# Optimization experiments

Measured on AMD Instinct MI355X. Metric: run time of the kernel, lower is better.

## Reference

```python
import jax, jax.numpy as jnp
import numpy as np
from jax import lax

CIN, COUT, NCLS = 512, 256, 1
B, H, W = 4, 64, 64
EPS = 1e-5


def conv1x1(x, w):
    # x: [B,I,H,W], w: [O,I]
    return jnp.einsum('oi,bihw->bohw', w, x)


def conv3x3(x, w):
    # x: [B,I,H,W], w: [O,I,3,3], padding=1
    return lax.conv_general_dilated(x, w, (1, 1), 'SAME',
                                    dimension_numbers=('NCHW', 'OIHW', 'NCHW'))


def bn_relu(x, g, b):
    # training-mode BatchNorm2d (biased var over B,H,W) + ReLU
    mean = jnp.mean(x, axis=(0, 2, 3), keepdims=True)
    var = jnp.var(x, axis=(0, 2, 3), keepdims=True)
    xn = (x - mean) * lax.rsqrt(var + EPS)
    return jax.nn.relu(xn * g[None, :, None, None] + b[None, :, None, None])


def attention(xf, yf, wq, wk, wv, gamma):
    # cross-attn when yf != xf, self-attn when yf is xf; no 1/sqrt(d) scaling (faithful)
    Bb, C, Hh, Ww = xf.shape
    N = Hh * Ww
    q = conv1x1(xf, wq).reshape(Bb, C, N)
    k = conv1x1(yf, wk).reshape(Bb, C, N)
    v = conv1x1(yf, wv).reshape(Bb, C, N)
    att = jax.nn.softmax(jnp.einsum('bcn,bcm->bnm', q, k), axis=-1)  # [B,N,N]
    out = jnp.einsum('bcm,bnm->bcn', v, att).reshape(Bb, C, Hh, Ww)  # v @ att^T
    return gamma * out + xf


def setup_inputs() -> dict:
    key = jax.random.key(0)
    ks = jax.random.split(key, 16)
    Cs = COUT + 2

    def w(k, shape, fan_in):
        return jax.random.normal(k, shape, dtype=jnp.float32) / np.sqrt(fan_in)

    return {
        'x': jax.random.normal(ks[0], (B, CIN, H, W), dtype=jnp.float32),
        'y': jax.random.normal(ks[1], (B, CIN, H, W), dtype=jnp.float32),
        'flow': jax.random.normal(ks[2], (B, 2, H, W), dtype=jnp.float32),
        'w1x1': w(ks[3], (COUT, CIN), CIN),
        'b1x1': jnp.zeros((COUT,), dtype=jnp.float32),
        'ca_wq': w(ks[4], (COUT, COUT), COUT),
        'ca_wk': w(ks[5], (COUT, COUT), COUT),
        'ca_wv': w(ks[6], (COUT, COUT), COUT),
        'ca_gamma': jnp.full((1,), 0.1, dtype=jnp.float32),
        'cbr1_w': w(ks[7], (COUT, COUT, 3, 3), COUT * 9),
        'bn1_g': jnp.ones((COUT,), dtype=jnp.float32),
        'bn1_b': jnp.zeros((COUT,), dtype=jnp.float32),
        'sa_wq': w(ks[8], (Cs, Cs), Cs),
        'sa_wk': w(ks[9], (Cs, Cs), Cs),
        'sa_wv': w(ks[10], (Cs, Cs), Cs),
        'sa_gamma': jnp.full((1,), 0.1, dtype=jnp.float32),
        'cbr2_w': w(ks[11], (COUT, Cs, 3, 3), Cs * 9),
        'bn2_g': jnp.ones((COUT,), dtype=jnp.float32),
        'bn2_b': jnp.zeros((COUT,), dtype=jnp.float32),
        'pred_w': w(ks[12], (NCLS, COUT), COUT),
        'pred_b': jnp.zeros((NCLS,), dtype=jnp.float32),
    }


def reference(x, y, flow, w1x1, b1x1, ca_wq, ca_wk, ca_wv, ca_gamma,
              cbr1_w, bn1_g, bn1_b, sa_wq, sa_wk, sa_wv, sa_gamma,
              cbr2_w, bn2_g, bn2_b, pred_w, pred_b):
    xb = conv1x1(x, w1x1) + b1x1[None, :, None, None]
    yb = conv1x1(y, w1x1) + b1x1[None, :, None, None]
    t = attention(xb, yb, ca_wq, ca_wk, ca_wv, ca_gamma)
    cross_out = bn_relu(conv3x3(t, cbr1_w), bn1_g, bn1_b)
    cat = jnp.concatenate([cross_out, flow], axis=1)  # [B, COUT+2, H, W]
    t = attention(cat, cat, sa_wq, sa_wk, sa_wv, sa_gamma)
    t = bn_relu(conv3x3(t, cbr2_w), bn2_g, bn2_b)
    out = conv1x1(t, pred_w) + pred_b[None, :, None, None]
    return out
```

## Files before the change

### kernel.cpp

```cpp
#include <hip/hip_runtime.h>
#include <hip/hip_bf16.h>
#include <math.h>


#define NPIX 4096
#define NB   4

typedef __attribute__((ext_vector_type(8))) short short8v;
typedef __attribute__((ext_vector_type(4))) float float4v;

__device__ __forceinline__ short f2bs(float f) {
  __hip_bfloat16 h = __float2bfloat16(f);
  short r; __builtin_memcpy(&r, &h, 2); return r;
}

__device__ __forceinline__ void glld16(const void* g, void* l) {
  __builtin_amdgcn_global_load_lds(
      (const __attribute__((address_space(1))) unsigned int*)g,
      (__attribute__((address_space(3))) unsigned int*)l, 16, 0, 0);
}

__global__ __launch_bounds__(256) void transp_kernel(
    const float* __restrict__ X, __hip_bfloat16* __restrict__ XT)
{
  const int i0 = blockIdx.x * 64, n0 = blockIdx.y * 64, b = blockIdx.z;
  const int tid = threadIdx.x;
  __shared__ float Ls[64][68];
#pragma unroll
  for (int it = 0; it < 4; ++it) {
    int ir = it * 16 + (tid >> 4);
    int nc = (tid & 15) * 4;
    float4 v = *(const float4*)(X + ((size_t)b * 512 + i0 + ir) * NPIX + n0 + nc);
    *(float4*)(&Ls[ir][nc]) = v;
  }
  __syncthreads();
#pragma unroll
  for (int ot = 0; ot < 2; ++ot) {
    int n = ot * 32 + (tid >> 3);
    int ig = tid & 7;
    short8v o;
#pragma unroll
    for (int j = 0; j < 8; ++j) o[j] = f2bs(Ls[8 * ig + j][n]);
    *(short8v*)(XT + ((size_t)b * NPIX + n0 + n) * 512 + i0 + 8 * ig) = o;
  }
}

__global__ void wprep_kernel(const float* __restrict__ Win,
                             __hip_bfloat16* __restrict__ Wout,
                             int Or, int Ir, int Op, int Ip)
{
  size_t total = (size_t)Op * Ip;
  for (size_t e = (size_t)blockIdx.x * 256 + threadIdx.x; e < total;
       e += (size_t)gridDim.x * 256) {
    int i = (int)(e % Ip);
    int o = (int)(e / Ip);
    float v = (o < Or && i < Ir) ? Win[(size_t)o * Ir + i] : 0.f;
    Wout[e] = __float2bfloat16(v);
  }
}

__global__ void wtransbf_kernel(const float* __restrict__ Win,
                                __hip_bfloat16* __restrict__ Wout,
                                int O, int Ir, int Ip)
{
  size_t total = (size_t)9 * O * Ip;
  for (size_t e = (size_t)blockIdx.x * 256 + threadIdx.x; e < total;
       e += (size_t)gridDim.x * 256) {
    int i = (int)(e % Ip);
    size_t r = e / Ip;
    int o = (int)(r % O);
    int dydx = (int)(r / O);
    float v = (i < Ir) ? Win[((size_t)o * Ir + i) * 9 + dydx] : 0.f;
    Wout[e] = __float2bfloat16(v);
  }
}

template<int OMODE>
__global__ __launch_bounds__(256, 3) void gemm3_kernel(
    const __hip_bfloat16* __restrict__ X, const __hip_bfloat16* __restrict__ Wb,
    const float* __restrict__ Bias, float* __restrict__ Yf,
    __hip_bfloat16* __restrict__ Yb, int Ip, int O)
{
  const int n0 = blockIdx.x * 64, o0 = blockIdx.y * 64, b = blockIdx.z;
  const int tid = threadIdx.x, wv = tid >> 6, lane = tid & 63;
  const int lg = lane >> 4, lr = lane & 15;
  __shared__ __align__(16) __hip_bfloat16 Xs[64 * 32];
  __shared__ __align__(16) __hip_bfloat16 Wsh[64 * 32];

  const int nn = tid >> 2, ig = tid & 3;
  const __hip_bfloat16* xrow = X + ((size_t)b * NPIX + n0 + nn) * Ip;
  const __hip_bfloat16* wrow = Wb + (size_t)(o0 + nn) * Ip;
  const int sw = 8 * (ig ^ (nn & 3));

  float4v acc[4];
#pragma unroll
  for (int f = 0; f < 4; ++f) acc[f] = (float4v){0.f, 0.f, 0.f, 0.f};

  const int nch = Ip >> 5;
  short8v xr_ = *(const short8v*)(xrow + sw);
  short8v wr_ = *(const short8v*)(wrow + sw);

  for (int ci = 0; ci < nch; ++ci) {
    __syncthreads();
    *(short8v*)(Xs  + nn * 32 + ig * 8) = xr_;
    *(short8v*)(Wsh + nn * 32 + ig * 8) = wr_;
    __syncthreads();
    if (ci + 1 < nch) {
      xr_ = *(const short8v*)(xrow + (ci + 1) * 32 + sw);
      wr_ = *(const short8v*)(wrow + (ci + 1) * 32 + sw);
    }
    if (OMODE != 4) {
      int ar = 16 * wv + lr;
      short8v a = *(const short8v*)(Xs + ar * 32 + 8 * (lg ^ (ar & 3)));
#pragma unroll
      for (int of = 0; of < 4; ++of) {
        int br = 16 * of + lr;
        short8v bb = *(const short8v*)(Wsh + br * 32 + 8 * (lg ^ (br & 3)));
        acc[of] = __builtin_amdgcn_mfma_f32_16x16x32_bf16(a, bb, acc[of], 0, 0, 0);
      }
    } else {
      int ar = 16 * wv + lr;
      short8v a = *(const short8v*)(Wsh + ar * 32 + 8 * (lg ^ (ar & 3)));
#pragma unroll
      for (int nf = 0; nf < 4; ++nf) {
        int br = 16 * nf + lr;
        short8v bb = *(const short8v*)(Xs + br * 32 + 8 * (lg ^ (br & 3)));
        acc[nf] = __builtin_amdgcn_mfma_f32_16x16x32_bf16(a, bb, acc[nf], 0, 0, 0);
      }
    }
  }

  if (OMODE < 2) {
#pragma unroll
    for (int r = 0; r < 4; ++r) {
      size_t row = (size_t)b * NPIX + n0 + 16 * wv + 4 * lg + r;
#pragma unroll
      for (int of = 0; of < 4; ++of) {
        int o = o0 + 16 * of + lr;
        if (o < O) {
          float v = acc[of][r] + (Bias ? Bias[o] : 0.f);
          if (OMODE == 0) Yf[row * O + o] = v;
          Yb[row * O + o] = __float2bfloat16(v);
        }
      }
    }
  } else if (OMODE == 3) {
    __hip_bfloat16* Hb = Yb + (size_t)b * NPIX * O;
#pragma unroll
    for (int r = 0; r < 4; ++r) {
      size_t n = n0 + 16 * wv + 4 * lg + r;
#pragma unroll
      for (int of = 0; of < 4; ++of) {
        int o = o0 + 16 * of + lr;
        if (o < O)
          Hb[((size_t)(o >> 3) * NPIX + n) * 8 + (o & 7)] = __float2bfloat16(acc[of][r]);
      }
    }
  } else {
    __hip_bfloat16* Hb = Yb + (size_t)b * NPIX * O;
#pragma unroll
    for (int r = 0; r < 4; ++r) {
      int c = o0 + 16 * wv + 4 * lg + r;
      if (c < O) {
#pragma unroll
        for (int nf = 0; nf < 4; ++nf) {
          int n = n0 + 16 * nf + lr;
          Hb[((size_t)(n >> 3) * O + c) * 8 + (n & 7)] = __float2bfloat16(acc[nf][r]);
        }
      }
    }
  }
}

template<int C, int RF, int S>
__global__ __launch_bounds__(256, 2) void flash4_kernel(
    const __hip_bfloat16* __restrict__ Q, const __hip_bfloat16* __restrict__ K,
    const __hip_bfloat16* __restrict__ V,
    __hip_bfloat16* __restrict__ Opart, float* __restrict__ ml)
{
  constexpr int N    = NPIX;
  constexpr int NC32 = C / 32;
  constexpr int NCF  = C / 16;
  constexpr int QB   = 16 * RF;
  constexpr int KBYTES = 128 * C;
  constexpr int NT   = (N / S) / 64;

  __shared__ __align__(1024) char smem[256 * C];
  __hip_bfloat16* Ks = (__hip_bfloat16*)smem;
  __hip_bfloat16* Vs = (__hip_bfloat16*)(smem + KBYTES);
  __hip_bfloat16* Ps = (__hip_bfloat16*)smem;

  const int n0 = blockIdx.x * (4 * QB);
  const int split = blockIdx.y, b = blockIdx.z;
  const int tid = threadIdx.x, w = tid >> 6, lane = tid & 63;
  const int lg = lane >> 4, lr = lane & 15;

  const __hip_bfloat16* Kb = K + (size_t)b * N * C;
  const __hip_bfloat16* Vb = V + (size_t)b * N * C;

  short8v qf[RF][NC32];
#pragma unroll
  for (int rf = 0; rf < RF; ++rf) {
    const __hip_bfloat16* qp =
        Q + ((size_t)b * N + n0 + QB * w + 16 * rf + lr) * C + 8 * lg;
#pragma unroll
    for (int ks = 0; ks < NC32; ++ks) qf[rf][ks] = *(const short8v*)(qp + 32 * ks);
  }

  float4v oacc[RF][NCF];
#pragma unroll
  for (int rf = 0; rf < RF; ++rf)
#pragma unroll
    for (int f = 0; f < NCF; ++f) oacc[rf][f] = (float4v){0.f, 0.f, 0.f, 0.f};
  float mrun[RF][4], lrun[RF][4];
#pragma unroll
  for (int rf = 0; rf < RF; ++rf)
#pragma unroll
    for (int r = 0; r < 4; ++r) { mrun[rf][r] = -INFINITY; lrun[rf][r] = 0.f; }

  const int m0base = split * (N / S);

  for (int t = 0; t < NT; ++t) {
    const int m0 = m0base + t * 64;
    __syncthreads();
    for (int u = w; u < C / 8; u += 4)
      glld16(Kb + ((size_t)u * N + m0 + lane) * 8, Ks + u * 512);
    for (int u = w; u < C / 8; u += 4) {
      int s = u * 64 + lane;
      int kv8 = s / C, c = s % C;
      glld16(Vb + ((size_t)(m0 / 8 + kv8) * C + c) * 8, Vs + u * 512);
    }
    asm volatile("s_waitcnt vmcnt(0)" ::: "memory");
    __syncthreads();

    float4v sacc[RF][4];
#pragma unroll
    for (int rf = 0; rf < RF; ++rf)
#pragma unroll
      for (int mf = 0; mf < 4; ++mf) sacc[rf][mf] = (float4v){0.f, 0.f, 0.f, 0.f};
    __builtin_amdgcn_s_setprio(1);
#pragma unroll
    for (int ks = 0; ks < NC32; ++ks)
#pragma unroll
      for (int mf = 0; mf < 4; ++mf) {
        short8v kf = *(const short8v*)(Ks + ((4 * ks + lg) * 64 + 16 * mf + lr) * 8);
#pragma unroll
        for (int rf = 0; rf < RF; ++rf)
          sacc[rf][mf] =
              __builtin_amdgcn_mfma_f32_16x16x32_bf16(qf[rf][ks], kf, sacc[rf][mf], 0, 0, 0);
      }
    __builtin_amdgcn_s_setprio(0);
    __syncthreads();

    float scal[RF][4];
#pragma unroll
    for (int rf = 0; rf < RF; ++rf)
#pragma unroll
      for (int r = 0; r < 4; ++r) {
        float pm = fmaxf(fmaxf(sacc[rf][0][r], sacc[rf][1][r]),
                         fmaxf(sacc[rf][2][r], sacc[rf][3][r]));
#pragma unroll
        for (int off = 1; off < 16; off <<= 1) pm = fmaxf(pm, __shfl_xor(pm, off));
        float mnew = fmaxf(mrun[rf][r], pm);
        float sc = __expf(mrun[rf][r] - mnew);
        mrun[rf][r] = mnew;
        float rs = 0.f;
#pragma unroll
        for (int mf = 0; mf < 4; ++mf) {
          float p = __expf(sacc[rf][mf][r] - mnew);
          rs += p;
          Ps[(size_t)(w * QB + 16 * rf + 4 * lg + r) * 72 + 16 * mf + lr] =
              __float2bfloat16(p);
        }
#pragma unroll
        for (int off = 1; off < 16; off <<= 1) rs += __shfl_xor(rs, off);
        lrun[rf][r] = lrun[rf][r] * sc + rs;
        scal[rf][r] = sc;
      }
#pragma unroll
    for (int rf = 0; rf < RF; ++rf)
#pragma unroll
      for (int f = 0; f < NCF; ++f)
#pragma unroll
        for (int r = 0; r < 4; ++r) oacc[rf][f][r] *= scal[rf][r];

    asm volatile("s_waitcnt lgkmcnt(0)" ::: "memory");

    short8v pa[RF][2];
#pragma unroll
    for (int rf = 0; rf < RF; ++rf)
#pragma unroll
      for (int h = 0; h < 2; ++h)
        pa[rf][h] = *(const short8v*)(Ps + (size_t)(w * QB + 16 * rf + lr) * 72 +
                                      32 * h + 8 * lg);
    __builtin_amdgcn_s_setprio(1);
#pragma unroll
    for (int cf = 0; cf < NCF; ++cf)
#pragma unroll
      for (int h = 0; h < 2; ++h) {
        short8v vf = *(const short8v*)(Vs + ((h * 4 + lg) * C + 16 * cf + lr) * 8);
#pragma unroll
        for (int rf = 0; rf < RF; ++rf)
          oacc[rf][cf] =
              __builtin_amdgcn_mfma_f32_16x16x32_bf16(pa[rf][h], vf, oacc[rf][cf], 0, 0, 0);
      }
    __builtin_amdgcn_s_setprio(0);
  }

  const size_t rbase = (size_t)(split * NB + b) * N;
#pragma unroll
  for (int rf = 0; rf < RF; ++rf)
#pragma unroll
    for (int r = 0; r < 4; ++r) {
      int n = n0 + QB * w + 16 * rf + 4 * lg + r;
      if (lr == 0) {
        ml[(rbase + n) * 2]     = mrun[rf][r];
        ml[(rbase + n) * 2 + 1] = lrun[rf][r];
      }
#pragma unroll
      for (int cf = 0; cf < NCF; ++cf)
        Opart[(rbase + n) * C + 16 * cf + lr] = __float2bfloat16(oacc[rf][cf][r]);
    }
}

template<int C, int S>
__global__ __launch_bounds__(256) void merge4_kernel(
    const __hip_bfloat16* __restrict__ Op, const float* __restrict__ ml,
    const float* __restrict__ R, const float* __restrict__ gamma_p,
    __hip_bfloat16* __restrict__ T)
{
  const size_t row = blockIdx.x;
  float m = -INFINITY;
#pragma unroll
  for (int s = 0; s < S; ++s)
    m = fmaxf(m, ml[((size_t)s * NB * NPIX + row) * 2]);
  float e[S]; float L = 0.f;
#pragma unroll
  for (int s = 0; s < S; ++s) {
    e[s] = __expf(ml[((size_t)s * NB * NPIX + row) * 2] - m);
    L += ml[((size_t)s * NB * NPIX + row) * 2 + 1] * e[s];
  }
  float rinv = gamma_p[0] / L;
  for (int c = threadIdx.x; c < C; c += 256) {
    float o = 0.f;
#pragma unroll
    for (int s = 0; s < S; ++s)
      o += __bfloat162float(Op[((size_t)s * NB * NPIX + row) * C + c]) * e[s];
    T[row * C + c] = __float2bfloat16(o * rinv + R[row * C + c]);
  }
}

template<int IC>
__global__ __launch_bounds__(256, 2) void conv3_kernel(
    const __hip_bfloat16* __restrict__ X, const __hip_bfloat16* __restrict__ W2,
    float* __restrict__ Y)
{
  constexpr int NCH = IC / 32;
  constexpr int XP = 66 * 32;
  const int h = blockIdx.x, o0 = blockIdx.y * 64, b = blockIdx.z;
  const int tid = threadIdx.x, wv = tid >> 6, lane = tid & 63;
  const int lg = lane >> 4, lr = lane & 15;

  __shared__ __align__(16) __hip_bfloat16 Ws[9 * 64 * 32];
  __shared__ __align__(16) __hip_bfloat16 X3[3 * XP];

  for (int e = tid; e < 192; e += 256) {
    int p = e / 64, rr = (e >> 5) & 1, i = e & 31;
    X3[p * XP + (rr ? 65 * 32 : 0) + i] = __float2bfloat16(0.f);
  }

  float4v acc[4];
#pragma unroll
  for (int f = 0; f < 4; ++f) acc[f] = (float4v){0.f, 0.f, 0.f, 0.f};

  short8v xreg[3], wreg[9];
#define LOADX(CI)                                                              \
  _Pragma("unroll")                                                            \
  for (int j = 0; j < 3; ++j) {                                                \
    int s = tid + j * 256;                                                     \
    int dy = s >> 8, ww = (s >> 2) & 63, ig = s & 3;                           \
    int hs = h + dy - 1;                                                       \
    if (hs >= 0 && hs < 64)                                                    \
      xreg[j] = *(const short8v*)(X + ((size_t)b * NPIX + hs * 64 + ww) * IC + \
                                  (CI) * 32 + 8 * (ig ^ ((ww + 1) & 3)));      \
    else                                                                       \
      xreg[j] = (short8v){0, 0, 0, 0, 0, 0, 0, 0};                             \
  }
#define LOADW(CI)                                                              \
  _Pragma("unroll")                                                            \
  for (int j = 0; j < 9; ++j) {                                                \
    int s = tid + j * 256;                                                     \
    int dydx = s >> 8, oo = (s >> 2) & 63, ig = s & 3;                         \
    wreg[j] = *(const short8v*)(W2 + ((size_t)(dydx * 256 + o0 + oo)) * IC +   \
                                (CI) * 32 + 8 * (ig ^ (oo & 3)));              \
  }
  LOADX(0); LOADW(0);

  for (int ci = 0; ci < NCH; ++ci) {
    __syncthreads();
#pragma unroll
    for (int j = 0; j < 3; ++j) {
      int s = tid + j * 256;
      int dy = s >> 8, ww = (s >> 2) & 63, ig = s & 3;
      *(short8v*)(X3 + dy * XP + (ww + 1) * 32 + ig * 8) = xreg[j];
    }
#pragma unroll
    for (int j = 0; j < 9; ++j) {
      int s = tid + j * 256;
      *(short8v*)(Ws + s * 8) = wreg[j];
    }
    __syncthreads();
    if (ci + 1 < NCH) { LOADX(ci + 1); LOADW(ci + 1); }
#pragma unroll
    for (int dy = 0; dy < 3; ++dy)
#pragma unroll
      for (int dx = 0; dx < 3; ++dx) {
        int rs_ = 16 * wv + lr + dx;
        short8v a = *(const short8v*)(X3 + dy * XP + rs_ * 32 + 8 * (lg ^ (rs_ & 3)));
#pragma unroll
        for (int of = 0; of < 4; ++of) {
          int br = 16 * of + lr;
          short8v bb = *(const short8v*)(Ws + (dy * 3 + dx) * 2048 + br * 32 +
                                         8 * (lg ^ (br & 3)));
          acc[of] = __builtin_amdgcn_mfma_f32_16x16x32_bf16(a, bb, acc[of], 0, 0, 0);
        }
      }
  }
#pragma unroll
  for (int r = 0; r < 4; ++r) {
    size_t row = (size_t)b * NPIX + h * 64 + 16 * wv + 4 * lg + r;
#pragma unroll
    for (int of = 0; of < 4; ++of)
      Y[row * 256 + o0 + 16 * of + lr] = acc[of][r];
  }
#undef LOADX
#undef LOADW
}

__global__ __launch_bounds__(256) void stats1_kernel(
    const float* __restrict__ X, float* __restrict__ Part)
{
  const int o0 = (blockIdx.x & 3) * 64;
  const int rc = blockIdx.x >> 2;
  const int tid = threadIdx.x;
  const int o = o0 + (tid & 63), rq = tid >> 6;
  float s = 0.f, sq = 0.f;
  for (int rr = rq; rr < 256; rr += 4) {
    float v = X[(size_t)(rc * 256 + rr) * 256 + o];
    s += v; sq += v * v;
  }
  __shared__ float rs[256], rq2[256];
  rs[tid] = s; rq2[tid] = sq;
  __syncthreads();
  if (tid < 64) {
    s  = rs[tid] + rs[tid + 64] + rs[tid + 128] + rs[tid + 192];
    sq = rq2[tid] + rq2[tid + 64] + rq2[tid + 128] + rq2[tid + 192];
    Part[(o0 + tid) * 128 + rc * 2]     = s;
    Part[(o0 + tid) * 128 + rc * 2 + 1] = sq;
  }
}

__global__ __launch_bounds__(256) void stats2_kernel(
    const float* __restrict__ Part, float* __restrict__ Mean, float* __restrict__ Rstd)
{
  const int o = threadIdx.x;
  float s = 0.f, sq = 0.f;
  for (int rc = 0; rc < 64; ++rc) {
    s += Part[o * 128 + rc * 2];
    sq += Part[o * 128 + rc * 2 + 1];
  }
  float mean = s / 16384.f;
  float var = sq / 16384.f - mean * mean;
  Mean[o] = mean;
  Rstd[o] = 1.f / sqrtf(var + 1e-5f);
}

__global__ __launch_bounds__(320) void bnapply1_kernel(
    const float* __restrict__ X, const float* __restrict__ Flow,
    const float* __restrict__ Mean, const float* __restrict__ Rstd,
    const float* __restrict__ G, const float* __restrict__ Bt,
    float* __restrict__ CatF, __hip_bfloat16* __restrict__ CatB)
{
  const size_t row = blockIdx.x;
  const int t = threadIdx.x;
  if (t >= 288) return;
  float val;
  if (t < 256) {
    float v = X[row * 256 + t];
    val = fmaxf((v - Mean[t]) * Rstd[t] * G[t] + Bt[t], 0.f);
  } else if (t < 258) {
    int b = (int)(row >> 12), n = (int)(row & 4095);
    val = Flow[((size_t)(b * 2 + (t - 256)) << 12) + n];
  } else val = 0.f;
  CatF[row * 288 + t] = val;
  CatB[row * 288 + t] = __float2bfloat16(val);
}

__global__ __launch_bounds__(256) void bnapply2_kernel(
    float* X, const float* __restrict__ Mean, const float* __restrict__ Rstd,
    const float* __restrict__ G, const float* __restrict__ Bt)
{
  const size_t idx = (size_t)blockIdx.x * 256 + threadIdx.x;
  const int t = threadIdx.x;
  float v = X[idx];
  X[idx] = fmaxf((v - Mean[t]) * Rstd[t] * G[t] + Bt[t], 0.f);
}

__global__ __launch_bounds__(256) void pred3_kernel(
    const float* __restrict__ X, const float* __restrict__ Wp,
    const float* __restrict__ Bp, float* __restrict__ Out)
{
  const int wv = threadIdx.x >> 6, lane = threadIdx.x & 63;
  const size_t row = (size_t)blockIdx.x * 4 + wv;
  const float* xr = X + row * 256;
  float acc = 0.f;
#pragma unroll
  for (int cc = 0; cc < 4; ++cc) acc = fmaf(xr[cc * 64 + lane], Wp[cc * 64 + lane], acc);
#pragma unroll
  for (int off = 1; off < 64; off <<= 1) acc += __shfl_xor(acc, off);
  if (lane == 0) Out[row] = acc + Bp[0];
}

extern "C" void kernel_launch(void* const* d_in, const int* in_sizes, int n_in,
                              void* d_out, int out_size, void* d_ws, size_t ws_size,
                              hipStream_t stream)
{
  (void)in_sizes; (void)n_in; (void)out_size; (void)ws_size;
  const float* x      = (const float*)d_in[0];
  const float* y      = (const float*)d_in[1];
  const float* flow   = (const float*)d_in[2];
  const float* w1x1   = (const float*)d_in[3];
  const float* b1x1   = (const float*)d_in[4];
  const float* ca_wq  = (const float*)d_in[5];
  const float* ca_wk  = (const float*)d_in[6];
  const float* ca_wv  = (const float*)d_in[7];
  const float* ca_g   = (const float*)d_in[8];
  const float* cbr1_w = (const float*)d_in[9];
  const float* bn1_g  = (const float*)d_in[10];
  const float* bn1_b  = (const float*)d_in[11];
  const float* sa_wq  = (const float*)d_in[12];
  const float* sa_wk  = (const float*)d_in[13];
  const float* sa_wv  = (const float*)d_in[14];
  const float* sa_g   = (const float*)d_in[15];
  const float* cbr2_w = (const float*)d_in[16];
  const float* bn2_g  = (const float*)d_in[17];
  const float* bn2_b  = (const float*)d_in[18];
  const float* pred_w = (const float*)d_in[19];
  const float* pred_b = (const float*)d_in[20];
  float* out = (float*)d_out;

  const size_t FSZ = (size_t)NB * NPIX * 288;
  const size_t SSZ = FSZ / 2;
  float* ws = (float*)d_ws;
  float* F0 = ws;
  float* F1 = ws + FSZ;
  float* F2 = ws + 2 * FSZ;
  float* Sb = ws + 3 * FSZ;
  __hip_bfloat16* S0 = (__hip_bfloat16*)(Sb);
  __hip_bfloat16* S1 = (__hip_bfloat16*)(Sb + SSZ);
  __hip_bfloat16* S2 = (__hip_bfloat16*)(Sb + 2 * SSZ);
  __hip_bfloat16* S3 = (__hip_bfloat16*)(Sb + 3 * SSZ);
  __hip_bfloat16* S4 = (__hip_bfloat16*)(Sb + 4 * SSZ);
  float* Wr = Sb + 5 * SSZ;
  __hip_bfloat16* w1bf  = (__hip_bfloat16*)Wr;
  __hip_bfloat16* caqb  = w1bf + (size_t)256 * 512;
  __hip_bfloat16* cakb  = caqb + (size_t)256 * 256;
  __hip_bfloat16* cavb  = cakb + (size_t)256 * 256;
  __hip_bfloat16* saqb  = cavb + (size_t)256 * 256;
  __hip_bfloat16* sakb  = saqb + (size_t)320 * 288;
  __hip_bfloat16* savb  = sakb + (size_t)320 * 288;
  __hip_bfloat16* w2abf = savb + (size_t)320 * 288;
  __hip_bfloat16* w2bbf = w2abf + (size_t)9 * 256 * 256;
  float* Part = (float*)(w2bbf + (size_t)9 * 256 * 288);
  float* Mean = Part + 32768;
  float* Rstd = Mean + 256;
  float* Mlb  = Rstd + 256;

  __hip_bfloat16* xT = (__hip_bfloat16*)F0;
  __hip_bfloat16* yT = (__hip_bfloat16*)F1;
  __hip_bfloat16* Op = (__hip_bfloat16*)F0;

  dim3 blk(256);

  wprep_kernel<<<dim3(256), blk, 0, stream>>>(w1x1, w1bf, 256, 512, 256, 512);
  wprep_kernel<<<dim3(256), blk, 0, stream>>>(ca_wq, caqb, 256, 256, 256, 256);
  wprep_kernel<<<dim3(256), blk, 0, stream>>>(ca_wk, cakb, 256, 256, 256, 256);
  wprep_kernel<<<dim3(256), blk, 0, stream>>>(ca_wv, cavb, 256, 256, 256, 256);
  wprep_kernel<<<dim3(256), blk, 0, stream>>>(sa_wq, saqb, 258, 258, 320, 288);
  wprep_kernel<<<dim3(256), blk, 0, stream>>>(sa_wk, sakb, 258, 258, 320, 288);
  wprep_kernel<<<dim3(256), blk, 0, stream>>>(sa_wv, savb, 258, 258, 320, 288);
  wtransbf_kernel<<<dim3(512), blk, 0, stream>>>(cbr1_w, w2abf, 256, 256, 256);
  wtransbf_kernel<<<dim3(512), blk, 0, stream>>>(cbr2_w, w2bbf, 256, 258, 288);

  transp_kernel<<<dim3(8, 64, 4), blk, 0, stream>>>(x, xT);
  transp_kernel<<<dim3(8, 64, 4), blk, 0, stream>>>(y, yT);

  gemm3_kernel<0><<<dim3(64, 4, 4), blk, 0, stream>>>(xT, w1bf, b1x1, F2, S0, 512, 256);
  gemm3_kernel<1><<<dim3(64, 4, 4), blk, 0, stream>>>(yT, w1bf, b1x1, nullptr, S1, 512, 256);

  gemm3_kernel<1><<<dim3(64, 4, 4), blk, 0, stream>>>(S0, caqb, nullptr, nullptr, S2, 256, 256);
  gemm3_kernel<3><<<dim3(64, 4, 4), blk, 0, stream>>>(S1, cakb, nullptr, nullptr, S3, 256, 256);
  gemm3_kernel<4><<<dim3(64, 4, 4), blk, 0, stream>>>(S1, cavb, nullptr, nullptr, S4, 256, 256);

  flash4_kernel<256, 2, 4><<<dim3(32, 4, 4), blk, 0, stream>>>(S2, S3, S4, Op, Mlb);
  merge4_kernel<256, 4><<<dim3(16384), blk, 0, stream>>>(Op, Mlb, F2, ca_g, S0);

  conv3_kernel<256><<<dim3(64, 4, 4), blk, 0, stream>>>(S0, w2abf, F0);
  stats1_kernel<<<dim3(256), blk, 0, stream>>>(F0, Part);
  stats2_kernel<<<dim3(1), blk, 0, stream>>>(Part, Mean, Rstd);
  bnapply1_kernel<<<dim3(16384), dim3(320), 0, stream>>>(F0, flow, Mean, Rstd,
                                                         bn1_g, bn1_b, F1, S3);

  gemm3_kernel<1><<<dim3(64, 5, 4), blk, 0, stream>>>(S3, saqb, nullptr, nullptr, S0, 288, 288);
  gemm3_kernel<3><<<dim3(64, 5, 4), blk, 0, stream>>>(S3, sakb, nullptr, nullptr, S1, 288, 288);
  gemm3_kernel<4><<<dim3(64, 5, 4), blk, 0, stream>>>(S3, savb, nullptr, nullptr, S2, 288, 288);

  flash4_kernel<288, 1, 2><<<dim3(64, 2, 4), blk, 0, stream>>>(S0, S1, S2, Op, Mlb);
  merge4_kernel<288, 2><<<dim3(16384), blk, 0, stream>>>(Op, Mlb, F1, sa_g, S4);

  conv3_kernel<288><<<dim3(64, 4, 4), blk, 0, stream>>>(S4, w2bbf, F0);
  stats1_kernel<<<dim3(256), blk, 0, stream>>>(F0, Part);
  stats2_kernel<<<dim3(1), blk, 0, stream>>>(Part, Mean, Rstd);
  bnapply2_kernel<<<dim3(16384), blk, 0, stream>>>(F0, Mean, Rstd, bn2_g, bn2_b);

  pred3_kernel<<<dim3(4096), blk, 0, stream>>>(F0, pred_w, pred_b, out);
}
```

Baseline: 545.0 us.

## Pipeline K/V loads in flash attention and double-buffer a 4-row conv3x3

The flash attention kernel now prefetches the next tile's K during softmax and the next V after the PV product, using split LDS buffers and finer waitcnt/barriers. It also adds a lazy-rescale path that skips the running-max update and accumulator rescale when the new tile max stays within 8 of the old one. Split counts change to 2 for both attentions, with 128 query rows per block and occupancy 1. The 3x3 conv now computes 4 output rows per block, staging input and weights with global_load_lds into double-buffered LDS, which increases weight reuse but raises register and LDS pressure.

```diff
diff --git a/kernel.cpp b/kernel.cpp
--- a/kernel.cpp
+++ b/kernel.cpp
@@ -18,6 +18,16 @@
   __builtin_amdgcn_global_load_lds(
       (const __attribute__((address_space(1))) unsigned int*)g,
       (__attribute__((address_space(3))) unsigned int*)l, 16, 0, 0);
+}
+
+__device__ __forceinline__ void vbar() { __builtin_amdgcn_s_barrier(); }
+__device__ __forceinline__ void waitlgkm() {
+  asm volatile("s_waitcnt lgkmcnt(0)" ::: "memory");
+}
+template<int NN> __device__ __forceinline__ void waitvm() {
+  if constexpr (NN == 0) asm volatile("s_waitcnt vmcnt(0)" ::: "memory");
+  else if constexpr (NN == 8) asm volatile("s_waitcnt vmcnt(8)" ::: "memory");
+  else if constexpr (NN == 9) asm volatile("s_waitcnt vmcnt(9)" ::: "memory");
 }
 
 __global__ __launch_bounds__(256) void transp_kernel(
@@ -172,8 +182,8 @@
   }
 }
 
-template<int C, int RF, int S>
-__global__ __launch_bounds__(256, 2) void flash4_kernel(
+template<int C>
+__global__ __launch_bounds__(256, 1) void flash5_kernel(
     const __hip_bfloat16* __restrict__ Q, const __hip_bfloat16* __restrict__ K,
     const __hip_bfloat16* __restrict__ V,
     __hip_bfloat16* __restrict__ Opart, float* __restrict__ ml)
@@ -181,16 +191,14 @@
   constexpr int N    = NPIX;
   constexpr int NC32 = C / 32;
   constexpr int NCF  = C / 16;
-  constexpr int QB   = 16 * RF;
-  constexpr int KBYTES = 128 * C;
-  constexpr int NT   = (N / S) / 64;
-
-  __shared__ __align__(1024) char smem[256 * C];
-  __hip_bfloat16* Ks = (__hip_bfloat16*)smem;
-  __hip_bfloat16* Vs = (__hip_bfloat16*)(smem + KBYTES);
-  __hip_bfloat16* Ps = (__hip_bfloat16*)smem;
-
-  const int n0 = blockIdx.x * (4 * QB);
+  constexpr int LVK  = C / 32;
+  constexpr int NT   = (N / 2) / 64;
+
+  __shared__ __align__(1024) __hip_bfloat16 Ks[64 * C];
+  __shared__ __align__(1024) __hip_bfloat16 Vs[64 * C];
+  __shared__ __align__(16)   __hip_bfloat16 Ps[4 * 32 * 72];
+
+  const int n0 = blockIdx.x * 128;
   const int split = blockIdx.y, b = blockIdx.z;
   const int tid = threadIdx.x, w = tid >> 6, lane = tid & 63;
   const int lg = lane >> 4, lr = lane & 15;
@@ -198,44 +206,53 @@
   const __hip_bfloat16* Kb = K + (size_t)b * N * C;
   const __hip_bfloat16* Vb = V + (size_t)b * N * C;
 
-  short8v qf[RF][NC32];
-#pragma unroll
-  for (int rf = 0; rf < RF; ++rf) {
+  short8v qf[2][NC32];
+#pragma unroll
+  for (int rf = 0; rf < 2; ++rf) {
     const __hip_bfloat16* qp =
-        Q + ((size_t)b * N + n0 + QB * w + 16 * rf + lr) * C + 8 * lg;
+        Q + ((size_t)b * N + n0 + 32 * w + 16 * rf + lr) * C + 8 * lg;
 #pragma unroll
     for (int ks = 0; ks < NC32; ++ks) qf[rf][ks] = *(const short8v*)(qp + 32 * ks);
   }
 
-  float4v oacc[RF][NCF];
-#pragma unroll
-  for (int rf = 0; rf < RF; ++rf)
+  float4v oacc[2][NCF];
+#pragma unroll
+  for (int rf = 0; rf < 2; ++rf)
 #pragma unroll
     for (int f = 0; f < NCF; ++f) oacc[rf][f] = (float4v){0.f, 0.f, 0.f, 0.f};
-  float mrun[RF][4], lrun[RF][4];
-#pragma unroll
-  for (int rf = 0; rf < RF; ++rf)
+  float mrun[2][4], lrun[2][4];
+#pragma unroll
+  for (int rf = 0; rf < 2; ++rf)
 #pragma unroll
     for (int r = 0; r < 4; ++r) { mrun[rf][r] = -INFINITY; lrun[rf][r] = 0.f; }
 
-  const int m0base = split * (N / S);
+  const int m0base = split * (N / 2);
+
+#define STAGEK(MM)                                                             \
+  _Pragma("unroll")                                                            \
+  for (int i = 0; i < LVK; ++i) {                                              \
+    int u = w + i * 4;                                                         \
+    glld16(Kb + ((size_t)u * N + (MM) + lane) * 8, Ks + u * 512);              \
+  }
+#define STAGEV(MM)                                                             \
+  _Pragma("unroll")                                                            \
+  for (int i = 0; i < LVK; ++i) {                                              \
+    int u = w + i * 4;                                                         \
+    int s = u * 64 + lane;                                                     \
+    int kv8 = s / C, c = s % C;                                                \
+    glld16(Vb + ((size_t)((MM) / 8 + kv8) * C + c) * 8, Vs + u * 512);         \
+  }
+
+  STAGEK(m0base);
+  STAGEV(m0base);
 
   for (int t = 0; t < NT; ++t) {
-    const int m0 = m0base + t * 64;
-    __syncthreads();
-    for (int u = w; u < C / 8; u += 4)
-      glld16(Kb + ((size_t)u * N + m0 + lane) * 8, Ks + u * 512);
-    for (int u = w; u < C / 8; u += 4) {
-      int s = u * 64 + lane;
-      int kv8 = s / C, c = s % C;
-      glld16(Vb + ((size_t)(m0 / 8 + kv8) * C + c) * 8, Vs + u * 512);
-    }
-    asm volatile("s_waitcnt vmcnt(0)" ::: "memory");
-    __syncthreads();
-
-    float4v sacc[RF][4];
-#pragma unroll
-    for (int rf = 0; rf < RF; ++rf)
+    const int mn = m0base + ((t + 1 == NT) ? 0 : (t + 1)) * 64;
+    waitvm<LVK>();
+    vbar();
+    float4v sacc[2][4];
+#pragma unroll
+    for (int rf = 0; rf < 2; ++rf)
 #pragma unroll
       for (int mf = 0; mf < 4; ++mf) sacc[rf][mf] = (float4v){0.f, 0.f, 0.f, 0.f};
     __builtin_amdgcn_s_setprio(1);
@@ -245,53 +262,87 @@
       for (int mf = 0; mf < 4; ++mf) {
         short8v kf = *(const short8v*)(Ks + ((4 * ks + lg) * 64 + 16 * mf + lr) * 8);
 #pragma unroll
-        for (int rf = 0; rf < RF; ++rf)
+        for (int rf = 0; rf < 2; ++rf)
           sacc[rf][mf] =
               __builtin_amdgcn_mfma_f32_16x16x32_bf16(qf[rf][ks], kf, sacc[rf][mf], 0, 0, 0);
       }
     __builtin_amdgcn_s_setprio(0);
-    __syncthreads();
-
-    float scal[RF][4];
-#pragma unroll
-    for (int rf = 0; rf < RF; ++rf)
+    waitlgkm();
+    vbar();
+    __builtin_amdgcn_sched_barrier(0);
+    STAGEK(mn);
+    float pm[2][4];
+#pragma unroll
+    for (int rf = 0; rf < 2; ++rf)
 #pragma unroll
       for (int r = 0; r < 4; ++r) {
-        float pm = fmaxf(fmaxf(sacc[rf][0][r], sacc[rf][1][r]),
-                         fmaxf(sacc[rf][2][r], sacc[rf][3][r]));
-#pragma unroll
-        for (int off = 1; off < 16; off <<= 1) pm = fmaxf(pm, __shfl_xor(pm, off));
-        float mnew = fmaxf(mrun[rf][r], pm);
-        float sc = __expf(mrun[rf][r] - mnew);
-        mrun[rf][r] = mnew;
-        float rs = 0.f;
-#pragma unroll
-        for (int mf = 0; mf < 4; ++mf) {
-          float p = __expf(sacc[rf][mf][r] - mnew);
-          rs += p;
-          Ps[(size_t)(w * QB + 16 * rf + 4 * lg + r) * 72 + 16 * mf + lr] =
-              __float2bfloat16(p);
+        float p = fmaxf(fmaxf(sacc[rf][0][r], sacc[rf][1][r]),
+                        fmaxf(sacc[rf][2][r], sacc[rf][3][r]));
+#pragma unroll
+        for (int off = 1; off < 16; off <<= 1) p = fmaxf(p, __shfl_xor(p, off));
+        pm[rf][r] = p;
+      }
+    int myok = 1;
+#pragma unroll
+    for (int rf = 0; rf < 2; ++rf)
+#pragma unroll
+      for (int r = 0; r < 4; ++r)
+        myok &= (pm[rf][r] <= mrun[rf][r] + 8.f) ? 1 : 0;
+    if (__all(myok)) {
+#pragma unroll
+      for (int rf = 0; rf < 2; ++rf)
+#pragma unroll
+        for (int r = 0; r < 4; ++r) {
+          float rs = 0.f;
+#pragma unroll
+          for (int mf = 0; mf < 4; ++mf) {
+            float p = __expf(sacc[rf][mf][r] - mrun[rf][r]);
+            rs += p;
+            Ps[(size_t)(w * 32 + 16 * rf + 4 * lg + r) * 72 + 16 * mf + lr] =
+                __float2bfloat16(p);
+          }
+#pragma unroll
+          for (int off = 1; off < 16; off <<= 1) rs += __shfl_xor(rs, off);
+          lrun[rf][r] += rs;
         }
-#pragma unroll
-        for (int off = 1; off < 16; off <<= 1) rs += __shfl_xor(rs, off);
-        lrun[rf][r] = lrun[rf][r] * sc + rs;
-        scal[rf][r] = sc;
-      }
-#pragma unroll
-    for (int rf = 0; rf < RF; ++rf)
-#pragma unroll
-      for (int f = 0; f < NCF; ++f)
-#pragma unroll
-        for (int r = 0; r < 4; ++r) oacc[rf][f][r] *= scal[rf][r];
-
-    asm volatile("s_waitcnt lgkmcnt(0)" ::: "memory");
-
-    short8v pa[RF][2];
-#pragma unroll
-    for (int rf = 0; rf < RF; ++rf)
+    } else {
+      float scal[2][4];
+#pragma unroll
+      for (int rf = 0; rf < 2; ++rf)
+#pragma unroll
+        for (int r = 0; r < 4; ++r) {
+          float mnew = fmaxf(mrun[rf][r], pm[rf][r]);
+          float sc = __expf(mrun[rf][r] - mnew);
+          mrun[rf][r] = mnew;
+          float rs = 0.f;
+#pragma unroll
+          for (int mf = 0; mf < 4; ++mf) {
+            float p = __expf(sacc[rf][mf][r] - mnew);
+            rs += p;
+            Ps[(size_t)(w * 32 + 16 * rf + 4 * lg + r) * 72 + 16 * mf + lr] =
+                __float2bfloat16(p);
+          }
+#pragma unroll
+          for (int off = 1; off < 16; off <<= 1) rs += __shfl_xor(rs, off);
+          lrun[rf][r] = lrun[rf][r] * sc + rs;
+          scal[rf][r] = sc;
+        }
+#pragma unroll
+      for (int rf = 0; rf < 2; ++rf)
+#pragma unroll
+        for (int f = 0; f < NCF; ++f)
+#pragma unroll
+          for (int r = 0; r < 4; ++r) oacc[rf][f][r] *= scal[rf][r];
+    }
+    waitlgkm();
+    waitvm<LVK>();
+    vbar();
+    short8v pa[2][2];
+#pragma unroll
+    for (int rf = 0; rf < 2; ++rf)
 #pragma unroll
       for (int h = 0; h < 2; ++h)
-        pa[rf][h] = *(const short8v*)(Ps + (size_t)(w * QB + 16 * rf + lr) * 72 +
+        pa[rf][h] = *(const short8v*)(Ps + (size_t)(w * 32 + 16 * rf + lr) * 72 +
                                       32 * h + 8 * lg);
     __builtin_amdgcn_s_setprio(1);
 #pragma unroll
@@ -300,19 +351,24 @@
       for (int h = 0; h < 2; ++h) {
         short8v vf = *(const short8v*)(Vs + ((h * 4 + lg) * C + 16 * cf + lr) * 8);
 #pragma unroll
-        for (int rf = 0; rf < RF; ++rf)
+        for (int rf = 0; rf < 2; ++rf)
           oacc[rf][cf] =
               __builtin_amdgcn_mfma_f32_16x16x32_bf16(pa[rf][h], vf, oacc[rf][cf], 0, 0, 0);
       }
     __builtin_amdgcn_s_setprio(0);
-  }
+    waitlgkm();
+    vbar();
+    STAGEV(mn);
+  }
+#undef STAGEK
+#undef STAGEV
 
   const size_t rbase = (size_t)(split * NB + b) * N;
 #pragma unroll
-  for (int rf = 0; rf < RF; ++rf)
+  for (int rf = 0; rf < 2; ++rf)
 #pragma unroll
     for (int r = 0; r < 4; ++r) {
-      int n = n0 + QB * w + 16 * rf + 4 * lg + r;
+      int n = n0 + 32 * w + 16 * rf + 4 * lg + r;
       if (lr == 0) {
         ml[(rbase + n) * 2]     = mrun[rf][r];
         ml[(rbase + n) * 2 + 1] = lrun[rf][r];
@@ -351,90 +407,116 @@
 }
 
 template<int IC>
-__global__ __launch_bounds__(256, 2) void conv3_kernel(
+__global__ __launch_bounds__(256, 1) void conv5_kernel(
     const __hip_bfloat16* __restrict__ X, const __hip_bfloat16* __restrict__ W2,
     float* __restrict__ Y)
 {
   constexpr int NCH = IC / 32;
   constexpr int XP = 66 * 32;
-  const int h = blockIdx.x, o0 = blockIdx.y * 64, b = blockIdx.z;
+  const int h0 = blockIdx.x * 4, o0 = blockIdx.y * 64, b = blockIdx.z;
   const int tid = threadIdx.x, wv = tid >> 6, lane = tid & 63;
   const int lg = lane >> 4, lr = lane & 15;
 
-  __shared__ __align__(16) __hip_bfloat16 Ws[9 * 64 * 32];
-  __shared__ __align__(16) __hip_bfloat16 X3[3 * XP];
-
-  for (int e = tid; e < 192; e += 256) {
-    int p = e / 64, rr = (e >> 5) & 1, i = e & 31;
-    X3[p * XP + (rr ? 65 * 32 : 0) + i] = __float2bfloat16(0.f);
-  }
-
-  float4v acc[4];
-#pragma unroll
-  for (int f = 0; f < 4; ++f) acc[f] = (float4v){0.f, 0.f, 0.f, 0.f};
-
-  short8v xreg[3], wreg[9];
-#define LOADX(CI)                                                              \
+  __shared__ __align__(1024) __hip_bfloat16 Xs[2][6 * XP];
+  __shared__ __align__(1024) __hip_bfloat16 Wsh[2][9 * 2048];
+
+  const __hip_bfloat16 zz = __float2bfloat16(0.f);
+  for (int e = tid; e < 384; e += 256) {
+    int p = e / 64, side = (e >> 5) & 1, ch = e & 31;
+    int sl = side ? 65 : 0;
+    Xs[0][p * XP + sl * 32 + ch] = zz;
+    Xs[1][p * XP + sl * 32 + ch] = zz;
+  }
+#pragma unroll
+  for (int p = 0; p < 6; ++p) {
+    int hs = h0 - 1 + p;
+    if (hs < 0 || hs > 63) {
+      for (int e = tid; e < XP; e += 256) {
+        Xs[0][p * XP + e] = zz;
+        Xs[1][p * XP + e] = zz;
+      }
+    }
+  }
+  __syncthreads();
+
+  float4v acc[4][4];
+#pragma unroll
+  for (int pf = 0; pf < 4; ++pf)
+#pragma unroll
+    for (int of = 0; of < 4; ++of) acc[pf][of] = (float4v){0.f, 0.f, 0.f, 0.f};
+
+#define CSTAGE(BUF, CI)                                                        \
   _Pragma("unroll")                                                            \
-  for (int j = 0; j < 3; ++j) {                                                \
-    int s = tid + j * 256;                                                     \
-    int dy = s >> 8, ww = (s >> 2) & 63, ig = s & 3;                           \
-    int hs = h + dy - 1;                                                       \
-    if (hs >= 0 && hs < 64)                                                    \
-      xreg[j] = *(const short8v*)(X + ((size_t)b * NPIX + hs * 64 + ww) * IC + \
-                                  (CI) * 32 + 8 * (ig ^ ((ww + 1) & 3)));      \
-    else                                                                       \
-      xreg[j] = (short8v){0, 0, 0, 0, 0, 0, 0, 0};                             \
-  }
-#define LOADW(CI)                                                              \
+  for (int k = 0; k < 6; ++k) {                                                \
+    int j = wv + k * 4;                                                        \
+    int p = j >> 2, seg = j & 3;                                               \
+    int hs = h0 - 1 + p;                                                       \
+    if (hs >= 0 && hs < 64) {                                                  \
+      int px = seg * 16 + (lane >> 2), ig = lane & 3;                          \
+      int sl = px + 1;                                                         \
+      glld16(X + ((size_t)(b * NPIX + hs * 64 + px)) * IC + (CI) * 32 +        \
+                 8 * (ig ^ (sl & 3)),                                          \
+             &Xs[BUF][p * XP + (1 + seg * 16) * 32]);                          \
+    }                                                                          \
+  }                                                                            \
   _Pragma("unroll")                                                            \
-  for (int j = 0; j < 9; ++j) {                                                \
-    int s = tid + j * 256;                                                     \
-    int dydx = s >> 8, oo = (s >> 2) & 63, ig = s & 3;                         \
-    wreg[j] = *(const short8v*)(W2 + ((size_t)(dydx * 256 + o0 + oo)) * IC +   \
-                                (CI) * 32 + 8 * (ig ^ (oo & 3)));              \
-  }
-  LOADX(0); LOADW(0);
-
+  for (int k = 0; k < 9; ++k) {                                                \
+    int j = wv + k * 4;                                                        \
+    int dydx = j >> 2, seg = j & 3;                                            \
+    int oo = seg * 16 + (lane >> 2), ig = lane & 3;                            \
+    glld16(W2 + ((size_t)(dydx * 256 + o0 + oo)) * IC + (CI) * 32 +            \
+               8 * (ig ^ (oo & 3)),                                            \
+           &Wsh[BUF][dydx * 2048 + seg * 512]);                                \
+  }
+
+  CSTAGE(0, 0);
+  int cur = 0;
   for (int ci = 0; ci < NCH; ++ci) {
-    __syncthreads();
-#pragma unroll
-    for (int j = 0; j < 3; ++j) {
-      int s = tid + j * 256;
-      int dy = s >> 8, ww = (s >> 2) & 63, ig = s & 3;
-      *(short8v*)(X3 + dy * XP + (ww + 1) * 32 + ig * 8) = xreg[j];
-    }
-#pragma unroll
-    for (int j = 0; j < 9; ++j) {
-      int s = tid + j * 256;
-      *(short8v*)(Ws + s * 8) = wreg[j];
-    }
-    __syncthreads();
-    if (ci + 1 < NCH) { LOADX(ci + 1); LOADW(ci + 1); }
-#pragma unroll
-    for (int dy = 0; dy < 3; ++dy)
+    asm volatile("s_waitcnt vmcnt(0) lgkmcnt(0)" ::: "memory");
+    vbar();
+    __builtin_amdgcn_sched_barrier(0);
+    const int cn = (ci + 1 == NCH) ? 0 : ci + 1;
+    if (cur) { CSTAGE(0, cn); } else { CSTAGE(1, cn); }
+    const __hip_bfloat16* xb = &Xs[cur][0];
+    const __hip_bfloat16* wb = &Wsh[cur][0];
+    __builtin_amdgcn_s_setprio(1);
+#pragma unroll
+    for (int dy = 0; dy < 3; ++dy) {
+      const __hip_bfloat16* xpl = xb + (wv + dy) * XP;
 #pragma unroll
       for (int dx = 0; dx < 3; ++dx) {
-        int rs_ = 16 * wv + lr + dx;
-        short8v a = *(const short8v*)(X3 + dy * XP + rs_ * 32 + 8 * (lg ^ (rs_ & 3)));
+        short8v a[4];
+#pragma unroll
+        for (int pf = 0; pf < 4; ++pf) {
+          int sl = pf * 16 + lr + dx;
+          a[pf] = *(const short8v*)(xpl + sl * 32 + 8 * (lg ^ (sl & 3)));
+        }
 #pragma unroll
         for (int of = 0; of < 4; ++of) {
           int br = 16 * of + lr;
-          short8v bb = *(const short8v*)(Ws + (dy * 3 + dx) * 2048 + br * 32 +
+          short8v bb = *(const short8v*)(wb + (dy * 3 + dx) * 2048 + br * 32 +
                                          8 * (lg ^ (br & 3)));
-          acc[of] = __builtin_amdgcn_mfma_f32_16x16x32_bf16(a, bb, acc[of], 0, 0, 0);
+#pragma unroll
+          for (int pf = 0; pf < 4; ++pf)
+            acc[pf][of] = __builtin_amdgcn_mfma_f32_16x16x32_bf16(a[pf], bb,
+                                                                  acc[pf][of], 0, 0, 0);
         }
       }
-  }
-#pragma unroll
-  for (int r = 0; r < 4; ++r) {
-    size_t row = (size_t)b * NPIX + h * 64 + 16 * wv + 4 * lg + r;
-#pragma unroll
-    for (int of = 0; of < 4; ++of)
-      Y[row * 256 + o0 + 16 * of + lr] = acc[of][r];
-  }
-#undef LOADX
-#undef LOADW
+    }
+    __builtin_amdgcn_s_setprio(0);
+    cur ^= 1;
+  }
+#undef CSTAGE
+
+#pragma unroll
+  for (int pf = 0; pf < 4; ++pf)
+#pragma unroll
+    for (int r = 0; r < 4; ++r) {
+      size_t row = (size_t)b * NPIX + (h0 + wv) * 64 + 16 * pf + 4 * lg + r;
+#pragma unroll
+      for (int of = 0; of < 4; ++of)
+        Y[row * 256 + o0 + 16 * of + lr] = acc[pf][of][r];
+    }
 }
 
 __global__ __launch_bounds__(256) void stats1_kernel(
@@ -602,10 +684,10 @@
   gemm3_kernel<3><<<dim3(64, 4, 4), blk, 0, stream>>>(S1, cakb, nullptr, nullptr, S3, 256, 256);
   gemm3_kernel<4><<<dim3(64, 4, 4), blk, 0, stream>>>(S1, cavb, nullptr, nullptr, S4, 256, 256);
 
-  flash4_kernel<256, 2, 4><<<dim3(32, 4, 4), blk, 0, stream>>>(S2, S3, S4, Op, Mlb);
-  merge4_kernel<256, 4><<<dim3(16384), blk, 0, stream>>>(Op, Mlb, F2, ca_g, S0);
-
-  conv3_kernel<256><<<dim3(64, 4, 4), blk, 0, stream>>>(S0, w2abf, F0);
+  flash5_kernel<256><<<dim3(32, 2, 4), blk, 0, stream>>>(S2, S3, S4, Op, Mlb);
+  merge4_kernel<256, 2><<<dim3(16384), blk, 0, stream>>>(Op, Mlb, F2, ca_g, S0);
+
+  conv5_kernel<256><<<dim3(16, 4, 4), blk, 0, stream>>>(S0, w2abf, F0);
   stats1_kernel<<<dim3(256), blk, 0, stream>>>(F0, Part);
   stats2_kernel<<<dim3(1), blk, 0, stream>>>(Part, Mean, Rstd);
   bnapply1_kernel<<<dim3(16384), dim3(320), 0, stream>>>(F0, flow, Mean, Rstd,
@@ -615,10 +697,10 @@
   gemm3_kernel<3><<<dim3(64, 5, 4), blk, 0, stream>>>(S3, sakb, nullptr, nullptr, S1, 288, 288);
   gemm3_kernel<4><<<dim3(64, 5, 4), blk, 0, stream>>>(S3, savb, nullptr, nullptr, S2, 288, 288);
 
-  flash4_kernel<288, 1, 2><<<dim3(64, 2, 4), blk, 0, stream>>>(S0, S1, S2, Op, Mlb);
+  flash5_kernel<288><<<dim3(32, 2, 4), blk, 0, stream>>>(S0, S1, S2, Op, Mlb);
   merge4_kernel<288, 2><<<dim3(16384), blk, 0, stream>>>(Op, Mlb, F1, sa_g, S4);
 
-  conv3_kernel<288><<<dim3(64, 4, 4), blk, 0, stream>>>(S4, w2bbf, F0);
+  conv5_kernel<288><<<dim3(16, 4, 4), blk, 0, stream>>>(S4, w2bbf, F0);
   stats1_kernel<<<dim3(256), blk, 0, stream>>>(F0, Part);
   stats2_kernel<<<dim3(1), blk, 0, stream>>>(Part, Mean, Rstd);
   bnapply2_kernel<<<dim3(16384), blk, 0, stream>>>(F0, Mean, Rstd, bn2_g, bn2_b);
```

Result: slower. 1.277 ms (+134.3%).

## Tile conv3x3 over four output rows with double-buffered direct-to-LDS loads

Applied to the files above, without the earlier changes.

Replaces the per-row conv3x3 kernel with one that computes four output rows per block. This reuses each weight tile across four times more pixels and shares halo rows. Staging now uses global_load_lds into double-buffered shared memory with a single barrier per channel chunk, instead of register-staged loads and two barriers. The grid shrinks to 256 blocks at one block per CU, which lowers occupancy and parallelism. Each thread also holds 16 accumulators, raising register pressure.

```diff
diff --git a/kernel.cpp b/kernel.cpp
--- a/kernel.cpp
+++ b/kernel.cpp
@@ -19,6 +19,8 @@
       (const __attribute__((address_space(1))) unsigned int*)g,
       (__attribute__((address_space(3))) unsigned int*)l, 16, 0, 0);
 }
+
+__device__ __forceinline__ void vbar() { __builtin_amdgcn_s_barrier(); }
 
 __global__ __launch_bounds__(256) void transp_kernel(
     const float* __restrict__ X, __hip_bfloat16* __restrict__ XT)
@@ -351,90 +353,116 @@
 }
 
 template<int IC>
-__global__ __launch_bounds__(256, 2) void conv3_kernel(
+__global__ __launch_bounds__(256, 1) void conv5_kernel(
     const __hip_bfloat16* __restrict__ X, const __hip_bfloat16* __restrict__ W2,
     float* __restrict__ Y)
 {
   constexpr int NCH = IC / 32;
   constexpr int XP = 66 * 32;
-  const int h = blockIdx.x, o0 = blockIdx.y * 64, b = blockIdx.z;
+  const int h0 = blockIdx.x * 4, o0 = blockIdx.y * 64, b = blockIdx.z;
   const int tid = threadIdx.x, wv = tid >> 6, lane = tid & 63;
   const int lg = lane >> 4, lr = lane & 15;
 
-  __shared__ __align__(16) __hip_bfloat16 Ws[9 * 64 * 32];
-  __shared__ __align__(16) __hip_bfloat16 X3[3 * XP];
-
-  for (int e = tid; e < 192; e += 256) {
-    int p = e / 64, rr = (e >> 5) & 1, i = e & 31;
-    X3[p * XP + (rr ? 65 * 32 : 0) + i] = __float2bfloat16(0.f);
-  }
-
-  float4v acc[4];
-#pragma unroll
-  for (int f = 0; f < 4; ++f) acc[f] = (float4v){0.f, 0.f, 0.f, 0.f};
-
-  short8v xreg[3], wreg[9];
-#define LOADX(CI)                                                              \
+  __shared__ __align__(1024) __hip_bfloat16 Xs[2][6 * XP];
+  __shared__ __align__(1024) __hip_bfloat16 Wsh[2][9 * 2048];
+
+  const __hip_bfloat16 zz = __float2bfloat16(0.f);
+  for (int e = tid; e < 384; e += 256) {
+    int p = e / 64, side = (e >> 5) & 1, ch = e & 31;
+    int sl = side ? 65 : 0;
+    Xs[0][p * XP + sl * 32 + ch] = zz;
+    Xs[1][p * XP + sl * 32 + ch] = zz;
+  }
+#pragma unroll
+  for (int p = 0; p < 6; ++p) {
+    int hs = h0 - 1 + p;
+    if (hs < 0 || hs > 63) {
+      for (int e = tid; e < XP; e += 256) {
+        Xs[0][p * XP + e] = zz;
+        Xs[1][p * XP + e] = zz;
+      }
+    }
+  }
+  __syncthreads();
+
+  float4v acc[4][4];
+#pragma unroll
+  for (int pf = 0; pf < 4; ++pf)
+#pragma unroll
+    for (int of = 0; of < 4; ++of) acc[pf][of] = (float4v){0.f, 0.f, 0.f, 0.f};
+
+#define CSTAGE(BUF, CI)                                                        \
   _Pragma("unroll")                                                            \
-  for (int j = 0; j < 3; ++j) {                                                \
-    int s = tid + j * 256;                                                     \
-    int dy = s >> 8, ww = (s >> 2) & 63, ig = s & 3;                           \
-    int hs = h + dy - 1;                                                       \
-    if (hs >= 0 && hs < 64)                                                    \
-      xreg[j] = *(const short8v*)(X + ((size_t)b * NPIX + hs * 64 + ww) * IC + \
-                                  (CI) * 32 + 8 * (ig ^ ((ww + 1) & 3)));      \
-    else                                                                       \
-      xreg[j] = (short8v){0, 0, 0, 0, 0, 0, 0, 0};                             \
-  }
-#define LOADW(CI)                                                              \
+  for (int k = 0; k < 6; ++k) {                                                \
+    int j = wv + k * 4;                                                        \
+    int p = j >> 2, seg = j & 3;                                               \
+    int hs = h0 - 1 + p;                                                       \
+    if (hs >= 0 && hs < 64) {                                                  \
+      int px = seg * 16 + (lane >> 2), ig = lane & 3;                          \
+      int sl = px + 1;                                                         \
+      glld16(X + ((size_t)(b * NPIX + hs * 64 + px)) * IC + (CI) * 32 +        \
+                 8 * (ig ^ (sl & 3)),                                          \
+             &Xs[BUF][p * XP + (1 + seg * 16) * 32]);                          \
+    }                                                                          \
+  }                                                                            \
   _Pragma("unroll")                                                            \
-  for (int j = 0; j < 9; ++j) {                                                \
-    int s = tid + j * 256;                                                     \
-    int dydx = s >> 8, oo = (s >> 2) & 63, ig = s & 3;                         \
-    wreg[j] = *(const short8v*)(W2 + ((size_t)(dydx * 256 + o0 + oo)) * IC +   \
-                                (CI) * 32 + 8 * (ig ^ (oo & 3)));              \
-  }
-  LOADX(0); LOADW(0);
-
+  for (int k = 0; k < 9; ++k) {                                                \
+    int j = wv + k * 4;                                                        \
+    int dydx = j >> 2, seg = j & 3;                                            \
+    int oo = seg * 16 + (lane >> 2), ig = lane & 3;                            \
+    glld16(W2 + ((size_t)(dydx * 256 + o0 + oo)) * IC + (CI) * 32 +            \
+               8 * (ig ^ (oo & 3)),                                            \
+           &Wsh[BUF][dydx * 2048 + seg * 512]);                                \
+  }
+
+  CSTAGE(0, 0);
+  int cur = 0;
   for (int ci = 0; ci < NCH; ++ci) {
-    __syncthreads();
-#pragma unroll
-    for (int j = 0; j < 3; ++j) {
-      int s = tid + j * 256;
-      int dy = s >> 8, ww = (s >> 2) & 63, ig = s & 3;
-      *(short8v*)(X3 + dy * XP + (ww + 1) * 32 + ig * 8) = xreg[j];
-    }
-#pragma unroll
-    for (int j = 0; j < 9; ++j) {
-      int s = tid + j * 256;
-      *(short8v*)(Ws + s * 8) = wreg[j];
-    }
-    __syncthreads();
-    if (ci + 1 < NCH) { LOADX(ci + 1); LOADW(ci + 1); }
-#pragma unroll
-    for (int dy = 0; dy < 3; ++dy)
+    asm volatile("s_waitcnt vmcnt(0) lgkmcnt(0)" ::: "memory");
+    vbar();
+    __builtin_amdgcn_sched_barrier(0);
+    const int cn = (ci + 1 == NCH) ? 0 : ci + 1;
+    if (cur) { CSTAGE(0, cn); } else { CSTAGE(1, cn); }
+    const __hip_bfloat16* xb = &Xs[cur][0];
+    const __hip_bfloat16* wb = &Wsh[cur][0];
+    __builtin_amdgcn_s_setprio(1);
+#pragma unroll
+    for (int dy = 0; dy < 3; ++dy) {
+      const __hip_bfloat16* xpl = xb + (wv + dy) * XP;
 #pragma unroll
       for (int dx = 0; dx < 3; ++dx) {
-        int rs_ = 16 * wv + lr + dx;
-        short8v a = *(const short8v*)(X3 + dy * XP + rs_ * 32 + 8 * (lg ^ (rs_ & 3)));
+        short8v a[4];
+#pragma unroll
+        for (int pf = 0; pf < 4; ++pf) {
+          int sl = pf * 16 + lr + dx;
+          a[pf] = *(const short8v*)(xpl + sl * 32 + 8 * (lg ^ (sl & 3)));
+        }
 #pragma unroll
         for (int of = 0; of < 4; ++of) {
           int br = 16 * of + lr;
-          short8v bb = *(const short8v*)(Ws + (dy * 3 + dx) * 2048 + br * 32 +
+          short8v bb = *(const short8v*)(wb + (dy * 3 + dx) * 2048 + br * 32 +
                                          8 * (lg ^ (br & 3)));
-          acc[of] = __builtin_amdgcn_mfma_f32_16x16x32_bf16(a, bb, acc[of], 0, 0, 0);
+#pragma unroll
+          for (int pf = 0; pf < 4; ++pf)
+            acc[pf][of] = __builtin_amdgcn_mfma_f32_16x16x32_bf16(a[pf], bb,
+                                                                  acc[pf][of], 0, 0, 0);
         }
       }
-  }
-#pragma unroll
-  for (int r = 0; r < 4; ++r) {
-    size_t row = (size_t)b * NPIX + h * 64 + 16 * wv + 4 * lg + r;
-#pragma unroll
-    for (int of = 0; of < 4; ++of)
-      Y[row * 256 + o0 + 16 * of + lr] = acc[of][r];
-  }
-#undef LOADX
-#undef LOADW
+    }
+    __builtin_amdgcn_s_setprio(0);
+    cur ^= 1;
+  }
+#undef CSTAGE
+
+#pragma unroll
+  for (int pf = 0; pf < 4; ++pf)
+#pragma unroll
+    for (int r = 0; r < 4; ++r) {
+      size_t row = (size_t)b * NPIX + (h0 + wv) * 64 + 16 * pf + 4 * lg + r;
+#pragma unroll
+      for (int of = 0; of < 4; ++of)
+        Y[row * 256 + o0 + 16 * of + lr] = acc[pf][of][r];
+    }
 }
 
 __global__ __launch_bounds__(256) void stats1_kernel(
@@ -605,7 +633,7 @@
   flash4_kernel<256, 2, 4><<<dim3(32, 4, 4), blk, 0, stream>>>(S2, S3, S4, Op, Mlb);
   merge4_kernel<256, 4><<<dim3(16384), blk, 0, stream>>>(Op, Mlb, F2, ca_g, S0);
 
-  conv3_kernel<256><<<dim3(64, 4, 4), blk, 0, stream>>>(S0, w2abf, F0);
+  conv5_kernel<256><<<dim3(16, 4, 4), blk, 0, stream>>>(S0, w2abf, F0);
   stats1_kernel<<<dim3(256), blk, 0, stream>>>(F0, Part);
   stats2_kernel<<<dim3(1), blk, 0, stream>>>(Part, Mean, Rstd);
   bnapply1_kernel<<<dim3(16384), dim3(320), 0, stream>>>(F0, flow, Mean, Rstd,
@@ -618,7 +646,7 @@
   flash4_kernel<288, 1, 2><<<dim3(64, 2, 4), blk, 0, stream>>>(S0, S1, S2, Op, Mlb);
   merge4_kernel<288, 2><<<dim3(16384), blk, 0, stream>>>(Op, Mlb, F1, sa_g, S4);
 
-  conv3_kernel<288><<<dim3(64, 4, 4), blk, 0, stream>>>(S4, w2bbf, F0);
+  conv5_kernel<288><<<dim3(16, 4, 4), blk, 0, stream>>>(S4, w2bbf, F0);
   stats1_kernel<<<dim3(256), blk, 0, stream>>>(F0, Part);
   stats2_kernel<<<dim3(1), blk, 0, stream>>>(Part, Mean, Rstd);
   bnapply2_kernel<<<dim3(16384), blk, 0, stream>>>(F0, Mean, Rstd, bn2_g, bn2_b);
```

Result: faster. 530.9 us (-2.6%).
